# Kernel optimization log

Measured on AMD Instinct MI355X. Metric: run time of the kernel, lower is better.

The kernel has to match this reference:

```python
import jax, jax.numpy as jnp
import numpy as np

N, E = 50000, 800000
IN_DIM, HIDDEN, OUT_DIM, LAYERS = 128, 64, 40, 3


def setup_inputs() -> dict:
    key = jax.random.key(0)
    ks = jax.random.split(key, 12)
    glorot = lambda k, fi, fo: jax.random.normal(k, (fi, fo), jnp.float32) * np.sqrt(2.0 / (fi + fo)).astype(np.float32)
    return {
        "x": jax.random.normal(ks[0], (N, IN_DIM), jnp.float32),
        "edge_index": jax.random.randint(ks[1], (2, E), 0, N, jnp.int64),
        "edge_weight": jax.random.uniform(ks[2], (E,), jnp.float32),
        "W1": glorot(ks[3], IN_DIM, HIDDEN), "b1": jnp.zeros((HIDDEN,), jnp.float32),
        "W2": glorot(ks[4], HIDDEN, HIDDEN), "b2": jnp.zeros((HIDDEN,), jnp.float32),
        "W3": glorot(ks[5], HIDDEN, HIDDEN), "b3": jnp.zeros((HIDDEN,), jnp.float32),
        "Wlin": glorot(ks[6], HIDDEN * LAYERS, OUT_DIM), "blin": jnp.zeros((OUT_DIM,), jnp.float32),
    }


def reference(x, edge_index, edge_weight, W1, b1, W2, b2, W3, b3, Wlin, blin):
    src, dst = edge_index[0], edge_index[1]

    def gcn_conv(h, W, b):
        # GCNConv with normalize=False: linear transform, then weighted sum aggregation at dst, then bias.
        h = h @ W                                   # [N, hidden]
        msg = h[src] * edge_weight[:, None]          # [E, hidden] gather + scale
        agg = jax.ops.segment_sum(msg, dst, num_segments=h.shape[0])  # scatter-add
        return agg + b

    outs = []
    h = x
    for W, b in ((W1, b1), (W2, b2), (W3, b3)):
        h = jax.nn.relu(gcn_conv(h, W, b))           # dropout is identity at inference
        outs.append(h)

    hjk = jnp.concatenate(outs, axis=-1)             # JumpingKnowledge mode='cat' -> [N, hidden*layers]
    return hjk @ Wlin + blin                         # [N, out_dim]
```

## Files before the change

kernel.cpp:

```cpp
#include <hip/hip_runtime.h>

#define HID 64
#define JK_DIM 192
#define OUT_DIM 40
#define AP 136
#define HP 72

typedef __attribute__((ext_vector_type(8))) short bf16x8;
typedef __attribute__((ext_vector_type(4))) float f32x4;

__device__ inline unsigned short f2b(float f) {
    unsigned u = __float_as_uint(f);
    unsigned r = u + 0x7FFF + ((u >> 16) & 1);
    return (unsigned short)(r >> 16);
}
__device__ inline float b2f(unsigned short u) {
    return __uint_as_float(((unsigned)u) << 16);
}
__device__ inline float blo(unsigned u) { return __uint_as_float(u << 16); }
__device__ inline float bhi(unsigned u) { return __uint_as_float(u & 0xFFFF0000u); }
__device__ inline unsigned pack2(float a, float b) {
    return (unsigned)f2b(a) | ((unsigned)f2b(b) << 16);
}

__global__ __launch_bounds__(256) void hist_dst(const int* __restrict__ dst,
                                                int* __restrict__ deg,
                                                unsigned short* __restrict__ rank,
                                                int E, int part, int histBlk,
                                                const float* __restrict__ W1,
                                                const float* __restrict__ W2,
                                                const float* __restrict__ W3,
                                                const float* __restrict__ Wlin,
                                                unsigned short* __restrict__ W1T,
                                                unsigned short* __restrict__ W2T,
                                                unsigned short* __restrict__ W3T,
                                                unsigned short* __restrict__ WlinT) {
    if ((int)blockIdx.x >= histBlk) {
        int base = (blockIdx.x - histBlk) * 256 + threadIdx.x;
        int stride = 32 * 256;
        for (int i = base; i < 64 * 128; i += stride) {
            int nn = i >> 7, k = i & 127;
            W1T[i] = f2b(W1[k * 64 + nn]);
        }
        for (int i = base; i < 64 * 64; i += stride) {
            int nn = i >> 6, k = i & 63;
            W2T[i] = f2b(W2[k * 64 + nn]);
            W3T[i] = f2b(W3[k * 64 + nn]);
        }
        for (int i = base; i < 48 * JK_DIM; i += stride) {
            int c = i / JK_DIM, k = i - c * JK_DIM;
            WlinT[i] = (c < OUT_DIM) ? f2b(Wlin[k * OUT_DIM + c]) : (unsigned short)0;
        }
        return;
    }
    int p = blockIdx.x & 7;
    int bid = blockIdx.x >> 3;
    int nblk = histBlk >> 3;
    int lo = p * part, hi = lo + part;
    int E4 = E >> 2;
    for (int q = bid * 256 + threadIdx.x; q < E4; q += nblk * 256) {
        int4 d4 = ((const int4*)dst)[q];
        int e = q * 4;
        if (d4.x >= lo && d4.x < hi) rank[e + 0] = (unsigned short)atomicAdd(&deg[d4.x], 1);
        if (d4.y >= lo && d4.y < hi) rank[e + 1] = (unsigned short)atomicAdd(&deg[d4.y], 1);
        if (d4.z >= lo && d4.z < hi) rank[e + 2] = (unsigned short)atomicAdd(&deg[d4.z], 1);
        if (d4.w >= lo && d4.w < hi) rank[e + 3] = (unsigned short)atomicAdd(&deg[d4.w], 1);
    }
    if (bid == 0 && threadIdx.x < (E & 3)) {
        int e = (E & ~3) + threadIdx.x;
        int d = dst[e];
        if (d >= lo && d < hi) rank[e] = (unsigned short)atomicAdd(&deg[d], 1);
    }
}

__global__ __launch_bounds__(256) void scan_fused(const int* __restrict__ deg,
                                                  int* __restrict__ off,
                                                  int* __restrict__ gctr, int n) {
    __shared__ int tmp[256];
    __shared__ int base;
    int i = blockIdx.x * 256 + threadIdx.x;
    int v = (i < n) ? deg[i] : 0;
    tmp[threadIdx.x] = v;
    __syncthreads();
    for (int d = 1; d < 256; d <<= 1) {
        int t = (threadIdx.x >= d) ? tmp[threadIdx.x - d] : 0;
        __syncthreads();
        tmp[threadIdx.x] += t;
        __syncthreads();
    }
    if (threadIdx.x == 255) base = atomicAdd(gctr, tmp[255]);
    __syncthreads();
    if (i < n) off[i] = base + tmp[threadIdx.x] - v;
}

__global__ __launch_bounds__(256) void fill_and_gemm(
        const int* __restrict__ src, const int* __restrict__ dst,
        const float* __restrict__ ew, const int* __restrict__ off,
        const unsigned short* __restrict__ rank,
        unsigned* __restrict__ ecsr, int E,
        const float* __restrict__ x, const unsigned short* __restrict__ W1T,
        unsigned short* __restrict__ linb, int n, int nFill) {
    __shared__ unsigned short Ah[64 * AP];
    __shared__ unsigned short Wt[64 * AP];
    int tid = threadIdx.x;
    if ((int)blockIdx.x < nFill) {
        int q = blockIdx.x * 256 + tid;
        int E4 = E >> 2;
        if (q < E4) {
            int4 d4 = ((const int4*)dst)[q];
            int4 s4 = ((const int4*)src)[q];
            float4 wv = ((const float4*)ew)[q];
            ushort4 r4 = ((const ushort4*)rank)[q];
            ecsr[off[d4.x] + r4.x] = (unsigned)s4.x | ((unsigned)f2b(wv.x) << 16);
            ecsr[off[d4.y] + r4.y] = (unsigned)s4.y | ((unsigned)f2b(wv.y) << 16);
            ecsr[off[d4.z] + r4.z] = (unsigned)s4.z | ((unsigned)f2b(wv.z) << 16);
            ecsr[off[d4.w] + r4.w] = (unsigned)s4.w | ((unsigned)f2b(wv.w) << 16);
        }
        if (blockIdx.x == 0 && tid < (E & 3)) {
            int e = (E & ~3) + tid;
            int d = dst[e];
            ecsr[off[d] + rank[e]] = (unsigned)src[e] | ((unsigned)f2b(ew[e]) << 16);
        }
        return;
    }
    int row0 = (blockIdx.x - nFill) * 64;
    if (row0 >= n) return;
    for (int i = tid; i < 64 * 32; i += 256) {
        int r = i >> 5;
        int c4 = (i & 31) * 4;
        int grow = row0 + r;
        if (grow >= n) grow = n - 1;
        float4 v = *(const float4*)(x + (long)grow * 128 + c4);
        ushort4 o;
        o.x = f2b(v.x); o.y = f2b(v.y); o.z = f2b(v.z); o.w = f2b(v.w);
        *(ushort4*)(Ah + r * AP + c4) = o;
    }
    for (int i = tid; i < 64 * 16; i += 256) {
        int nn = i >> 4;
        int k8 = (i & 15) * 8;
        *(uint4*)(Wt + nn * AP + k8) = *(const uint4*)(W1T + nn * 128 + k8);
    }
    __syncthreads();

    int wave = tid >> 6;
    int lane = tid & 63;
    int lr = lane & 15;
    int lk = (lane >> 4) * 8;
    f32x4 acc[4];
#pragma unroll
    for (int nf = 0; nf < 4; ++nf) acc[nf] = (f32x4){0.f, 0.f, 0.f, 0.f};
#pragma unroll
    for (int k0 = 0; k0 < 128; k0 += 32) {
        bf16x8 a = *(const bf16x8*)(Ah + (wave * 16 + lr) * AP + k0 + lk);
#pragma unroll
        for (int nf = 0; nf < 4; ++nf) {
            bf16x8 b = *(const bf16x8*)(Wt + (nf * 16 + lr) * AP + k0 + lk);
            acc[nf] = __builtin_amdgcn_mfma_f32_16x16x32_bf16(a, b, acc[nf], 0, 0, 0);
        }
    }
    int mbase = wave * 16 + (lane >> 4) * 4;
#pragma unroll
    for (int nf = 0; nf < 4; ++nf) {
#pragma unroll
        for (int r = 0; r < 4; ++r) {
            int grow = row0 + mbase + r;
            if (grow < n)
                linb[(long)grow * HID + nf * 16 + lr] = f2b(acc[nf][r]);
        }
    }
}

__global__ __launch_bounds__(256) void aggregate(const unsigned short* __restrict__ linb,
                                                 const unsigned* __restrict__ ecsr,
                                                 const int* __restrict__ off,
                                                 const int* __restrict__ deg,
                                                 const float* __restrict__ bias,
                                                 unsigned short* __restrict__ hout, int n) {
    int cl = threadIdx.x & 7;
    float4 bLo = *(const float4*)(bias + cl * 8);
    float4 bHi = *(const float4*)(bias + cl * 8 + 4);
    int grp = (blockIdx.x * 256 + threadIdx.x) >> 3;
    int ngrp = (gridDim.x * 256) >> 3;
    for (int node = grp; node < n; node += ngrp) {
        int start = off[node];
        int cnt = deg[node];
        float acc[8];
#pragma unroll
        for (int i = 0; i < 8; ++i) acc[i] = 0.f;

        int s[8];
        float w[8];
#pragma unroll
        for (int t = 0; t < 8; ++t) {
            s[t] = 0; w[t] = 0.f;
            if (t < cnt) {
                unsigned m = ecsr[start + t];
                s[t] = (int)(m & 0xFFFFu);
                w[t] = b2f((unsigned short)(m >> 16));
            }
        }
        for (int bb = 0; bb < cnt; bb += 8) {
            int s2[8];
            float w2[8];
#pragma unroll
            for (int t = 0; t < 8; ++t) {
                int e = bb + 8 + t;
                s2[t] = 0; w2[t] = 0.f;
                if (e < cnt) {
                    unsigned m = ecsr[start + e];
                    s2[t] = (int)(m & 0xFFFFu);
                    w2[t] = b2f((unsigned short)(m >> 16));
                }
            }
            uint4 u[8];
#pragma unroll
            for (int t = 0; t < 8; ++t)
                u[t] = *(const uint4*)(linb + (long)s[t] * HID + cl * 8);
#pragma unroll
            for (int t = 0; t < 8; ++t) {
                acc[0] += blo(u[t].x) * w[t];
                acc[1] += bhi(u[t].x) * w[t];
                acc[2] += blo(u[t].y) * w[t];
                acc[3] += bhi(u[t].y) * w[t];
                acc[4] += blo(u[t].z) * w[t];
                acc[5] += bhi(u[t].z) * w[t];
                acc[6] += blo(u[t].w) * w[t];
                acc[7] += bhi(u[t].w) * w[t];
            }
#pragma unroll
            for (int t = 0; t < 8; ++t) { s[t] = s2[t]; w[t] = w2[t]; }
        }

        uint4 o;
        o.x = pack2(fmaxf(acc[0] + bLo.x, 0.f), fmaxf(acc[1] + bLo.y, 0.f));
        o.y = pack2(fmaxf(acc[2] + bLo.z, 0.f), fmaxf(acc[3] + bLo.w, 0.f));
        o.z = pack2(fmaxf(acc[4] + bHi.x, 0.f), fmaxf(acc[5] + bHi.y, 0.f));
        o.w = pack2(fmaxf(acc[6] + bHi.z, 0.f), fmaxf(acc[7] + bHi.w, 0.f));
        *(uint4*)(hout + (long)node * JK_DIM + cl * 8) = o;
    }
}

__global__ __launch_bounds__(256) void agg_transform(
        const unsigned short* __restrict__ hprev,
        const unsigned* __restrict__ ecsr,
        const int* __restrict__ off, const int* __restrict__ deg,
        const unsigned short* __restrict__ WT, const float* __restrict__ bias,
        unsigned short* __restrict__ hout, int n) {
    __shared__ unsigned short Hs[64 * HP];
    __shared__ unsigned short Wt[64 * HP];
    int tid = threadIdx.x;
    int row0 = blockIdx.x * 64;
    if (row0 >= n) return;
    for (int i = tid; i < 64 * 8; i += 256) {
        int nn = i >> 3;
        int k8 = (i & 7) * 8;
        *(uint4*)(Wt + nn * HP + k8) = *(const uint4*)(WT + nn * 64 + k8);
    }
    int cl = tid & 7;
    int g0 = tid >> 3;
    for (int gi = 0; gi < 2; ++gi) {
        int lrow = g0 + gi * 32;
        int node = row0 + lrow;
        float acc[8];
#pragma unroll
        for (int i = 0; i < 8; ++i) acc[i] = 0.f;
        if (node < n) {
            int start = off[node];
            int cnt = deg[node];
            int s[8];
            float w[8];
#pragma unroll
            for (int t = 0; t < 8; ++t) {
                s[t] = 0; w[t] = 0.f;
                if (t < cnt) {
                    unsigned m = ecsr[start + t];
                    s[t] = (int)(m & 0xFFFFu);
                    w[t] = b2f((unsigned short)(m >> 16));
                }
            }
            for (int bb = 0; bb < cnt; bb += 8) {
                int s2[8];
                float w2[8];
#pragma unroll
                for (int t = 0; t < 8; ++t) {
                    int e = bb + 8 + t;
                    s2[t] = 0; w2[t] = 0.f;
                    if (e < cnt) {
                        unsigned m = ecsr[start + e];
                        s2[t] = (int)(m & 0xFFFFu);
                        w2[t] = b2f((unsigned short)(m >> 16));
                    }
                }
                uint4 u[8];
#pragma unroll
                for (int t = 0; t < 8; ++t)
                    u[t] = *(const uint4*)(hprev + (long)s[t] * JK_DIM + cl * 8);
#pragma unroll
                for (int t = 0; t < 8; ++t) {
                    acc[0] += blo(u[t].x) * w[t];
                    acc[1] += bhi(u[t].x) * w[t];
                    acc[2] += blo(u[t].y) * w[t];
                    acc[3] += bhi(u[t].y) * w[t];
                    acc[4] += blo(u[t].z) * w[t];
                    acc[5] += bhi(u[t].z) * w[t];
                    acc[6] += blo(u[t].w) * w[t];
                    acc[7] += bhi(u[t].w) * w[t];
                }
#pragma unroll
                for (int t = 0; t < 8; ++t) { s[t] = s2[t]; w[t] = w2[t]; }
            }
        }
        uint4 o;
        o.x = pack2(acc[0], acc[1]);
        o.y = pack2(acc[2], acc[3]);
        o.z = pack2(acc[4], acc[5]);
        o.w = pack2(acc[6], acc[7]);
        *(uint4*)(Hs + lrow * HP + cl * 8) = o;
    }
    __syncthreads();
    int wave = tid >> 6;
    int lane = tid & 63;
    int lr = lane & 15;
    int lk = (lane >> 4) * 8;
    f32x4 d[4];
#pragma unroll
    for (int nf = 0; nf < 4; ++nf) d[nf] = (f32x4){0.f, 0.f, 0.f, 0.f};
#pragma unroll
    for (int k0 = 0; k0 < 64; k0 += 32) {
        bf16x8 a = *(const bf16x8*)(Hs + (wave * 16 + lr) * HP + k0 + lk);
#pragma unroll
        for (int nf = 0; nf < 4; ++nf) {
            bf16x8 b = *(const bf16x8*)(Wt + (nf * 16 + lr) * HP + k0 + lk);
            d[nf] = __builtin_amdgcn_mfma_f32_16x16x32_bf16(a, b, d[nf], 0, 0, 0);
        }
    }
    int mbase = wave * 16 + (lane >> 4) * 4;
#pragma unroll
    for (int nf = 0; nf < 4; ++nf) {
        float bv = bias[nf * 16 + lr];
#pragma unroll
        for (int r = 0; r < 4; ++r) {
            int grow = row0 + mbase + r;
            if (grow < n)
                hout[(long)grow * JK_DIM + nf * 16 + lr] = f2b(fmaxf(d[nf][r] + bv, 0.f));
        }
    }
}

__global__ __launch_bounds__(256) void jk_final(
        const unsigned short* __restrict__ hprev,
        const unsigned* __restrict__ ecsr,
        const int* __restrict__ off, const int* __restrict__ deg,
        const unsigned short* __restrict__ W3T, const float* __restrict__ bias,
        const unsigned short* __restrict__ hcat,
        const unsigned short* __restrict__ WlinT,
        const float* __restrict__ blin,
        float* __restrict__ outp, int n) {
    __shared__ unsigned short pool[128 * HP];
    unsigned short* Hs = pool;
    unsigned short* Wt = pool + 64 * HP;
    int tid = threadIdx.x;
    int row0 = blockIdx.x * 64;
    if (row0 >= n) return;
    for (int i = tid; i < 64 * 8; i += 256) {
        int nn = i >> 3;
        int k8 = (i & 7) * 8;
        *(uint4*)(Wt + nn * HP + k8) = *(const uint4*)(W3T + nn * 64 + k8);
    }
    int cl = tid & 7;
    int g0 = tid >> 3;
    for (int gi = 0; gi < 2; ++gi) {
        int lrow = g0 + gi * 32;
        int node = row0 + lrow;
        float acc[8];
#pragma unroll
        for (int i = 0; i < 8; ++i) acc[i] = 0.f;
        if (node < n) {
            int start = off[node];
            int cnt = deg[node];
            int s[8];
            float w[8];
#pragma unroll
            for (int t = 0; t < 8; ++t) {
                s[t] = 0; w[t] = 0.f;
                if (t < cnt) {
                    unsigned m = ecsr[start + t];
                    s[t] = (int)(m & 0xFFFFu);
                    w[t] = b2f((unsigned short)(m >> 16));
                }
            }
            for (int bb = 0; bb < cnt; bb += 8) {
                int s2[8];
                float w2[8];
#pragma unroll
                for (int t = 0; t < 8; ++t) {
                    int e = bb + 8 + t;
                    s2[t] = 0; w2[t] = 0.f;
                    if (e < cnt) {
                        unsigned m = ecsr[start + e];
                        s2[t] = (int)(m & 0xFFFFu);
                        w2[t] = b2f((unsigned short)(m >> 16));
                    }
                }
                uint4 u[8];
#pragma unroll
                for (int t = 0; t < 8; ++t)
                    u[t] = *(const uint4*)(hprev + (long)s[t] * JK_DIM + cl * 8);
#pragma unroll
                for (int t = 0; t < 8; ++t) {
                    acc[0] += blo(u[t].x) * w[t];
                    acc[1] += bhi(u[t].x) * w[t];
                    acc[2] += blo(u[t].y) * w[t];
                    acc[3] += bhi(u[t].y) * w[t];
                    acc[4] += blo(u[t].z) * w[t];
                    acc[5] += bhi(u[t].z) * w[t];
                    acc[6] += blo(u[t].w) * w[t];
                    acc[7] += bhi(u[t].w) * w[t];
                }
#pragma unroll
                for (int t = 0; t < 8; ++t) { s[t] = s2[t]; w[t] = w2[t]; }
            }
        }
        uint4 o;
        o.x = pack2(acc[0], acc[1]);
        o.y = pack2(acc[2], acc[3]);
        o.z = pack2(acc[4], acc[5]);
        o.w = pack2(acc[6], acc[7]);
        *(uint4*)(Hs + lrow * HP + cl * 8) = o;
    }
    __syncthreads();
    int wave = tid >> 6;
    int lane = tid & 63;
    int lr = lane & 15;
    int lk = (lane >> 4) * 8;
    f32x4 d[4];
#pragma unroll
    for (int nf = 0; nf < 4; ++nf) d[nf] = (f32x4){0.f, 0.f, 0.f, 0.f};
#pragma unroll
    for (int k0 = 0; k0 < 64; k0 += 32) {
        bf16x8 a = *(const bf16x8*)(Hs + (wave * 16 + lr) * HP + k0 + lk);
#pragma unroll
        for (int nf = 0; nf < 4; ++nf) {
            bf16x8 b = *(const bf16x8*)(Wt + (nf * 16 + lr) * HP + k0 + lk);
            d[nf] = __builtin_amdgcn_mfma_f32_16x16x32_bf16(a, b, d[nf], 0, 0, 0);
        }
    }
    int mbase = wave * 16 + (lane >> 4) * 4;
    unsigned short* As = Hs;
    unsigned short* WL = Wt;
    f32x4 acc2[3];
#pragma unroll
    for (int nf = 0; nf < 3; ++nf) acc2[nf] = (f32x4){0.f, 0.f, 0.f, 0.f};
    for (int ch = 0; ch < 2; ++ch) {
        int cb = ch * 64;
        __syncthreads();
        for (int i = tid; i < 64 * 8; i += 256) {
            int r = i >> 3;
            int q8 = (i & 7) * 8;
            int grow = row0 + r;
            if (grow >= n) grow = n - 1;
            *(uint4*)(As + r * HP + q8) = *(const uint4*)(hcat + (long)grow * JK_DIM + cb + q8);
        }
        for (int i = tid; i < 48 * 8; i += 256) {
            int c = i >> 3;
            int k8 = (i & 7) * 8;
            *(uint4*)(WL + c * HP + k8) = *(const uint4*)(WlinT + c * JK_DIM + cb + k8);
        }
        __syncthreads();
#pragma unroll
        for (int k0 = 0; k0 < 64; k0 += 32) {
            bf16x8 a = *(const bf16x8*)(As + (wave * 16 + lr) * HP + k0 + lk);
#pragma unroll
            for (int nf = 0; nf < 3; ++nf) {
                bf16x8 b = *(const bf16x8*)(WL + (nf * 16 + lr) * HP + k0 + lk);
                acc2[nf] = __builtin_amdgcn_mfma_f32_16x16x32_bf16(a, b, acc2[nf], 0, 0, 0);
            }
        }
    }
    __syncthreads();
#pragma unroll
    for (int nf = 0; nf < 4; ++nf) {
        float bv = bias[nf * 16 + lr];
#pragma unroll
        for (int r = 0; r < 4; ++r)
            As[(mbase + r) * HP + nf * 16 + lr] = f2b(fmaxf(d[nf][r] + bv, 0.f));
    }
    for (int i = tid; i < 48 * 8; i += 256) {
        int c = i >> 3;
        int k8 = (i & 7) * 8;
        *(uint4*)(WL + c * HP + k8) = *(const uint4*)(WlinT + c * JK_DIM + 128 + k8);
    }
    __syncthreads();
#pragma unroll
    for (int k0 = 0; k0 < 64; k0 += 32) {
        bf16x8 a = *(const bf16x8*)(As + (wave * 16 + lr) * HP + k0 + lk);
#pragma unroll
        for (int nf = 0; nf < 3; ++nf) {
            bf16x8 b = *(const bf16x8*)(WL + (nf * 16 + lr) * HP + k0 + lk);
            acc2[nf] = __builtin_amdgcn_mfma_f32_16x16x32_bf16(a, b, acc2[nf], 0, 0, 0);
        }
    }
#pragma unroll
    for (int nf = 0; nf < 3; ++nf) {
        int col = nf * 16 + lr;
        if (col < OUT_DIM) {
            float bb = blin[col];
#pragma unroll
            for (int r = 0; r < 4; ++r) {
                int grow = row0 + mbase + r;
                if (grow < n)
                    outp[(long)grow * OUT_DIM + col] = acc2[nf][r] + bb;
            }
        }
    }
}

extern "C" void kernel_launch(void* const* d_in, const int* in_sizes, int n_in,
                              void* d_out, int out_size, void* d_ws, size_t ws_size,
                              hipStream_t stream) {
    const float* x    = (const float*)d_in[0];
    const int*   ei   = (const int*)d_in[1];
    const float* ew   = (const float*)d_in[2];
    const float* W1   = (const float*)d_in[3];
    const float* b1   = (const float*)d_in[4];
    const float* W2   = (const float*)d_in[5];
    const float* b2   = (const float*)d_in[6];
    const float* W3   = (const float*)d_in[7];
    const float* b3   = (const float*)d_in[8];
    const float* Wlin = (const float*)d_in[9];
    const float* blin = (const float*)d_in[10];
    float* out = (float*)d_out;

    const int N = in_sizes[0] / 128;
    const int E = in_sizes[2];
    const int* src = ei;
    const int* dst = ei + E;
    const int PART = (N + 7) / 8;

    char* wsb = (char*)d_ws;
    unsigned short* linb  = (unsigned short*)wsb;   wsb += (long)N * HID * 2;
    unsigned short* hcatb = (unsigned short*)wsb;   wsb += (long)N * JK_DIM * 2;
    char* zbase = wsb;
    int* deg    = (int*)wsb;                        wsb += (long)N * 4;
    int* off    = (int*)wsb;                        wsb += (long)N * 4;
    int* bsum   = (int*)wsb;                        wsb += 256 * 4;
    size_t zbytes = (size_t)(wsb - zbase);
    unsigned short* W1T  = (unsigned short*)wsb;    wsb += 64 * 128 * 2;
    unsigned short* W2T  = (unsigned short*)wsb;    wsb += 64 * 64 * 2;
    unsigned short* W3T  = (unsigned short*)wsb;    wsb += 64 * 64 * 2;
    unsigned short* WlinT = (unsigned short*)wsb;   wsb += 48 * JK_DIM * 2;
    unsigned* ecsr = (unsigned*)wsb;
    unsigned short* rank = hcatb;
    int* gctr = bsum;

    dim3 blk(256);
    const int nblkN = (N + 255) / 256;
    dim3 gN(nblkN);
    const int histBlk = 8 * 104;
    dim3 gHist(histBlk + 32);
    const int nFill = ((E >> 2) + 255) / 256;
    const int nGemm = (N + 63) / 64;
    dim3 gFG(nFill + nGemm);
    dim3 gTile((N + 63) / 64);
    dim3 gAgg((N + 31) / 32);

    unsigned short* h1 = hcatb;
    unsigned short* h2 = hcatb + HID;

    hipMemsetAsync(zbase, 0, zbytes, stream);

    hist_dst<<<gHist, blk, 0, stream>>>(dst, deg, rank, E, PART, histBlk,
                                        W1, W2, W3, Wlin, W1T, W2T, W3T, WlinT);
    scan_fused<<<gN, blk, 0, stream>>>(deg, off, gctr, N);

    fill_and_gemm<<<gFG, blk, 0, stream>>>(src, dst, ew, off, rank, ecsr, E,
                                           x, W1T, linb, N, nFill);
    aggregate<<<gAgg, blk, 0, stream>>>(linb, ecsr, off, deg, b1, h1, N);

    agg_transform<<<gTile, blk, 0, stream>>>(h1, ecsr, off, deg, W2T, b2, h2, N);

    jk_final<<<gTile, blk, 0, stream>>>(h2, ecsr, off, deg, W3T, b3,
                                        hcatb, WlinT, blin, out, N);
}
```

Measured before the change: 229.9 us.

## Move layer-1 GEMM into histogram kernel and split CSR fill out

The first-layer x@W1 GEMM blocks now run in the same launch as the destination histogram instead of alongside the CSR fill. Each GEMM block reads fp32 W1 directly and transposes it into shared memory, so the separate W1T conversion is no longer needed. The CSR fill becomes its own small kernel after the scan. The aim is to overlap the compute-heavy GEMM with the atomic-bound histogram. The cost is heavier shared-memory use in the histogram launch, which may lower its occupancy, plus a strided transposed LDS write in every GEMM block.

```diff
diff --git a/kernel.cpp b/kernel.cpp
--- a/kernel.cpp
+++ b/kernel.cpp
@@ -23,25 +23,23 @@
     return (unsigned)f2b(a) | ((unsigned)f2b(b) << 16);
 }
 
-__global__ __launch_bounds__(256) void hist_dst(const int* __restrict__ dst,
-                                                int* __restrict__ deg,
-                                                unsigned short* __restrict__ rank,
-                                                int E, int part, int histBlk,
-                                                const float* __restrict__ W1,
-                                                const float* __restrict__ W2,
-                                                const float* __restrict__ W3,
-                                                const float* __restrict__ Wlin,
-                                                unsigned short* __restrict__ W1T,
-                                                unsigned short* __restrict__ W2T,
-                                                unsigned short* __restrict__ W3T,
-                                                unsigned short* __restrict__ WlinT) {
-    if ((int)blockIdx.x >= histBlk) {
-        int base = (blockIdx.x - histBlk) * 256 + threadIdx.x;
+__global__ __launch_bounds__(256) void hist_gemm(
+        const int* __restrict__ dst, int* __restrict__ deg,
+        unsigned short* __restrict__ rank, int E, int part,
+        int nGemm, int histBlk,
+        const float* __restrict__ x, const float* __restrict__ W1,
+        unsigned short* __restrict__ linb, int n,
+        const float* __restrict__ W2, const float* __restrict__ W3,
+        const float* __restrict__ Wlin,
+        unsigned short* __restrict__ W2T, unsigned short* __restrict__ W3T,
+        unsigned short* __restrict__ WlinT) {
+    __shared__ unsigned short Ah[64 * AP];
+    __shared__ unsigned short Wt[64 * AP];
+    int tid = threadIdx.x;
+    int bid = blockIdx.x;
+    if (bid >= nGemm + histBlk) {
+        int base = (bid - nGemm - histBlk) * 256 + tid;
         int stride = 32 * 256;
-        for (int i = base; i < 64 * 128; i += stride) {
-            int nn = i >> 7, k = i & 127;
-            W1T[i] = f2b(W1[k * 64 + nn]);
-        }
         for (int i = base; i < 64 * 64; i += stride) {
             int nn = i >> 6, k = i & 63;
             W2T[i] = f2b(W2[k * 64 + nn]);
@@ -53,77 +51,29 @@
         }
         return;
     }
-    int p = blockIdx.x & 7;
-    int bid = blockIdx.x >> 3;
-    int nblk = histBlk >> 3;
-    int lo = p * part, hi = lo + part;
-    int E4 = E >> 2;
-    for (int q = bid * 256 + threadIdx.x; q < E4; q += nblk * 256) {
-        int4 d4 = ((const int4*)dst)[q];
-        int e = q * 4;
-        if (d4.x >= lo && d4.x < hi) rank[e + 0] = (unsigned short)atomicAdd(&deg[d4.x], 1);
-        if (d4.y >= lo && d4.y < hi) rank[e + 1] = (unsigned short)atomicAdd(&deg[d4.y], 1);
-        if (d4.z >= lo && d4.z < hi) rank[e + 2] = (unsigned short)atomicAdd(&deg[d4.z], 1);
-        if (d4.w >= lo && d4.w < hi) rank[e + 3] = (unsigned short)atomicAdd(&deg[d4.w], 1);
-    }
-    if (bid == 0 && threadIdx.x < (E & 3)) {
-        int e = (E & ~3) + threadIdx.x;
-        int d = dst[e];
-        if (d >= lo && d < hi) rank[e] = (unsigned short)atomicAdd(&deg[d], 1);
-    }
-}
-
-__global__ __launch_bounds__(256) void scan_fused(const int* __restrict__ deg,
-                                                  int* __restrict__ off,
-                                                  int* __restrict__ gctr, int n) {
-    __shared__ int tmp[256];
-    __shared__ int base;
-    int i = blockIdx.x * 256 + threadIdx.x;
-    int v = (i < n) ? deg[i] : 0;
-    tmp[threadIdx.x] = v;
-    __syncthreads();
-    for (int d = 1; d < 256; d <<= 1) {
-        int t = (threadIdx.x >= d) ? tmp[threadIdx.x - d] : 0;
-        __syncthreads();
-        tmp[threadIdx.x] += t;
-        __syncthreads();
-    }
-    if (threadIdx.x == 255) base = atomicAdd(gctr, tmp[255]);
-    __syncthreads();
-    if (i < n) off[i] = base + tmp[threadIdx.x] - v;
-}
-
-__global__ __launch_bounds__(256) void fill_and_gemm(
-        const int* __restrict__ src, const int* __restrict__ dst,
-        const float* __restrict__ ew, const int* __restrict__ off,
-        const unsigned short* __restrict__ rank,
-        unsigned* __restrict__ ecsr, int E,
-        const float* __restrict__ x, const unsigned short* __restrict__ W1T,
-        unsigned short* __restrict__ linb, int n, int nFill) {
-    __shared__ unsigned short Ah[64 * AP];
-    __shared__ unsigned short Wt[64 * AP];
-    int tid = threadIdx.x;
-    if ((int)blockIdx.x < nFill) {
-        int q = blockIdx.x * 256 + tid;
+    if (bid >= nGemm) {
+        int hb = bid - nGemm;
+        int p = hb & 7;
+        int hbid = hb >> 3;
+        int nblk = histBlk >> 3;
+        int lo = p * part, hi = lo + part;
         int E4 = E >> 2;
-        if (q < E4) {
+        for (int q = hbid * 256 + tid; q < E4; q += nblk * 256) {
             int4 d4 = ((const int4*)dst)[q];
-            int4 s4 = ((const int4*)src)[q];
-            float4 wv = ((const float4*)ew)[q];
-            ushort4 r4 = ((const ushort4*)rank)[q];
-            ecsr[off[d4.x] + r4.x] = (unsigned)s4.x | ((unsigned)f2b(wv.x) << 16);
-            ecsr[off[d4.y] + r4.y] = (unsigned)s4.y | ((unsigned)f2b(wv.y) << 16);
-            ecsr[off[d4.z] + r4.z] = (unsigned)s4.z | ((unsigned)f2b(wv.z) << 16);
-            ecsr[off[d4.w] + r4.w] = (unsigned)s4.w | ((unsigned)f2b(wv.w) << 16);
-        }
-        if (blockIdx.x == 0 && tid < (E & 3)) {
+            int e = q * 4;
+            if (d4.x >= lo && d4.x < hi) rank[e + 0] = (unsigned short)atomicAdd(&deg[d4.x], 1);
+            if (d4.y >= lo && d4.y < hi) rank[e + 1] = (unsigned short)atomicAdd(&deg[d4.y], 1);
+            if (d4.z >= lo && d4.z < hi) rank[e + 2] = (unsigned short)atomicAdd(&deg[d4.z], 1);
+            if (d4.w >= lo && d4.w < hi) rank[e + 3] = (unsigned short)atomicAdd(&deg[d4.w], 1);
+        }
+        if (hbid == 0 && tid < (E & 3)) {
             int e = (E & ~3) + tid;
             int d = dst[e];
-            ecsr[off[d] + rank[e]] = (unsigned)src[e] | ((unsigned)f2b(ew[e]) << 16);
+            if (d >= lo && d < hi) rank[e] = (unsigned short)atomicAdd(&deg[d], 1);
         }
         return;
     }
-    int row0 = (blockIdx.x - nFill) * 64;
+    int row0 = bid * 64;
     if (row0 >= n) return;
     for (int i = tid; i < 64 * 32; i += 256) {
         int r = i >> 5;
@@ -135,10 +85,14 @@
         o.x = f2b(v.x); o.y = f2b(v.y); o.z = f2b(v.z); o.w = f2b(v.w);
         *(ushort4*)(Ah + r * AP + c4) = o;
     }
-    for (int i = tid; i < 64 * 16; i += 256) {
-        int nn = i >> 4;
-        int k8 = (i & 15) * 8;
-        *(uint4*)(Wt + nn * AP + k8) = *(const uint4*)(W1T + nn * 128 + k8);
+    for (int i = tid; i < 128 * 16; i += 256) {
+        int k = i >> 4;
+        int n4 = (i & 15) * 4;
+        float4 v = *(const float4*)(W1 + (long)k * 64 + n4);
+        Wt[(n4 + 0) * AP + k] = f2b(v.x);
+        Wt[(n4 + 1) * AP + k] = f2b(v.y);
+        Wt[(n4 + 2) * AP + k] = f2b(v.z);
+        Wt[(n4 + 3) * AP + k] = f2b(v.w);
     }
     __syncthreads();
 
@@ -167,6 +121,51 @@
             if (grow < n)
                 linb[(long)grow * HID + nf * 16 + lr] = f2b(acc[nf][r]);
         }
+    }
+}
+
+__global__ __launch_bounds__(256) void scan_fused(const int* __restrict__ deg,
+                                                  int* __restrict__ off,
+                                                  int* __restrict__ gctr, int n) {
+    __shared__ int tmp[256];
+    __shared__ int base;
+    int i = blockIdx.x * 256 + threadIdx.x;
+    int v = (i < n) ? deg[i] : 0;
+    tmp[threadIdx.x] = v;
+    __syncthreads();
+    for (int d = 1; d < 256; d <<= 1) {
+        int t = (threadIdx.x >= d) ? tmp[threadIdx.x - d] : 0;
+        __syncthreads();
+        tmp[threadIdx.x] += t;
+        __syncthreads();
+    }
+    if (threadIdx.x == 255) base = atomicAdd(gctr, tmp[255]);
+    __syncthreads();
+    if (i < n) off[i] = base + tmp[threadIdx.x] - v;
+}
+
+__global__ __launch_bounds__(256) void fill_csr(
+        const int* __restrict__ src, const int* __restrict__ dst,
+        const float* __restrict__ ew, const int* __restrict__ off,
+        const unsigned short* __restrict__ rank,
+        unsigned* __restrict__ ecsr, int E) {
+    int tid = threadIdx.x;
+    int q = blockIdx.x * 256 + tid;
+    int E4 = E >> 2;
+    if (q < E4) {
+        int4 d4 = ((const int4*)dst)[q];
+        int4 s4 = ((const int4*)src)[q];
+        float4 wv = ((const float4*)ew)[q];
+        ushort4 r4 = ((const ushort4*)rank)[q];
+        ecsr[off[d4.x] + r4.x] = (unsigned)s4.x | ((unsigned)f2b(wv.x) << 16);
+        ecsr[off[d4.y] + r4.y] = (unsigned)s4.y | ((unsigned)f2b(wv.y) << 16);
+        ecsr[off[d4.z] + r4.z] = (unsigned)s4.z | ((unsigned)f2b(wv.z) << 16);
+        ecsr[off[d4.w] + r4.w] = (unsigned)s4.w | ((unsigned)f2b(wv.w) << 16);
+    }
+    if (blockIdx.x == 0 && tid < (E & 3)) {
+        int e = (E & ~3) + tid;
+        int d = dst[e];
+        ecsr[off[d] + rank[e]] = (unsigned)src[e] | ((unsigned)f2b(ew[e]) << 16);
     }
 }
 
@@ -545,7 +544,6 @@
     int* off    = (int*)wsb;                        wsb += (long)N * 4;
     int* bsum   = (int*)wsb;                        wsb += 256 * 4;
     size_t zbytes = (size_t)(wsb - zbase);
-    unsigned short* W1T  = (unsigned short*)wsb;    wsb += 64 * 128 * 2;
     unsigned short* W2T  = (unsigned short*)wsb;    wsb += 64 * 64 * 2;
     unsigned short* W3T  = (unsigned short*)wsb;    wsb += 64 * 64 * 2;
     unsigned short* WlinT = (unsigned short*)wsb;   wsb += 48 * JK_DIM * 2;
@@ -556,11 +554,11 @@
     dim3 blk(256);
     const int nblkN = (N + 255) / 256;
     dim3 gN(nblkN);
+    const int nGemm = (N + 63) / 64;
     const int histBlk = 8 * 104;
-    dim3 gHist(histBlk + 32);
+    dim3 gHG(nGemm + histBlk + 32);
     const int nFill = ((E >> 2) + 255) / 256;
-    const int nGemm = (N + 63) / 64;
-    dim3 gFG(nFill + nGemm);
+    dim3 gFill(nFill);
     dim3 gTile((N + 63) / 64);
     dim3 gAgg((N + 31) / 32);
 
@@ -569,16 +567,14 @@
 
     hipMemsetAsync(zbase, 0, zbytes, stream);
 
-    hist_dst<<<gHist, blk, 0, stream>>>(dst, deg, rank, E, PART, histBlk,
-                                        W1, W2, W3, Wlin, W1T, W2T, W3T, WlinT);
+    hist_gemm<<<gHG, blk, 0, stream>>>(dst, deg, rank, E, PART, nGemm, histBlk,
+                                       x, W1, linb, N, W2, W3, Wlin,
+                                       W2T, W3T, WlinT);
     scan_fused<<<gN, blk, 0, stream>>>(deg, off, gctr, N);
-
-    fill_and_gemm<<<gFG, blk, 0, stream>>>(src, dst, ew, off, rank, ecsr, E,
-                                           x, W1T, linb, N, nFill);
+    fill_csr<<<gFill, blk, 0, stream>>>(src, dst, ew, off, rank, ecsr, E);
+
     aggregate<<<gAgg, blk, 0, stream>>>(linb, ecsr, off, deg, b1, h1, N);
-
     agg_transform<<<gTile, blk, 0, stream>>>(h1, ecsr, off, deg, W2T, b2, h2, N);
-
     jk_final<<<gTile, blk, 0, stream>>>(h2, ecsr, off, deg, W3T, b3,
                                         hcatb, WlinT, blin, out, N);
 }
```

Result: no change. 228.5 us, median of 2 (-0.6%).
